# Performance work log

Measured on AMD Instinct MI355X. Metric: run time of the kernel, lower is better.

The kernel has to match this reference:

```python
import jax, jax.numpy as jnp
import numpy as np
import math

D_MODEL = 1024
NUM_HEADS = 16
HEAD_DIM = D_MODEL // NUM_HEADS
BATCH = 2
SEQ = 2048
THETA = 10000.0


def _rope_tables(seq_len, head_dim, theta=THETA):
    inv_freq = 1.0 / theta ** (jnp.arange(0, head_dim, 2, dtype=jnp.float32) / head_dim)
    pos = jnp.arange(seq_len, dtype=jnp.float32)
    freqs = jnp.outer(pos, inv_freq)                 # [S, hd/2]
    emb = jnp.concatenate([freqs, freqs], axis=-1)   # [S, hd]
    return jnp.cos(emb), jnp.sin(emb)


def _rotate_half(x):
    x1, x2 = jnp.split(x, 2, axis=-1)
    return jnp.concatenate([-x2, x1], axis=-1)


def setup_inputs() -> dict:
    key = jax.random.key(0)
    k1, k2, k3 = jax.random.split(key, 3)
    x = jax.random.normal(k1, (BATCH, SEQ, D_MODEL), dtype=jnp.float32)
    # causal mask: 1 where attend allowed, 0 where masked
    mask = jnp.tril(jnp.ones((SEQ, SEQ), dtype=jnp.int32))[None, None]
    w_qkv = jax.random.normal(k2, (D_MODEL, 3 * D_MODEL), dtype=jnp.float32) / math.sqrt(D_MODEL)
    w_out = jax.random.normal(k3, (D_MODEL, D_MODEL), dtype=jnp.float32) / math.sqrt(D_MODEL)
    return {"x": x, "mask": mask, "w_qkv": w_qkv, "w_out": w_out}


def reference(x, mask, w_qkv, w_out):
    B, S, _ = x.shape
    qkv = x @ w_qkv                                          # [B,S,3*D]
    qkv = qkv.reshape(B, S, 3, NUM_HEADS, HEAD_DIM)
    qkv = jnp.transpose(qkv, (2, 0, 3, 1, 4))                # [3,B,H,S,hd]
    q, k, v = qkv[0], qkv[1], qkv[2]
    cos, sin = _rope_tables(S, HEAD_DIM)                     # [S,hd]
    cos = cos[None, None]; sin = sin[None, None]
    q = q * cos + _rotate_half(q) * sin
    k = k * cos + _rotate_half(k) * sin
    scores = jnp.einsum('bhqd,bhkd->bhqk', q, k) / math.sqrt(HEAD_DIM)
    scores = jnp.where(mask == 0, -jnp.inf, scores)
    attn = jax.nn.softmax(scores, axis=-1)                   # dropout p=0 (eval)
    out = jnp.einsum('bhqk,bhkd->bhqd', attn, v)             # [B,H,S,hd]
    out = jnp.transpose(out, (0, 2, 1, 3)).reshape(B, S, D_MODEL)
    return out @ w_out
```

## Files before the change

### kernel.cpp

```cpp
#include <hip/hip_runtime.h>

typedef __bf16 bf16;
typedef __bf16 bf16x4 __attribute__((ext_vector_type(4)));
typedef __bf16 bf16x8 __attribute__((ext_vector_type(8)));
typedef short s16x4 __attribute__((ext_vector_type(4)));
typedef float f32x4 __attribute__((ext_vector_type(4)));

constexpr int BATCH = 2;
constexpr int SEQ   = 2048;
constexpr int DMODEL= 1024;
constexpr int NH    = 16;
constexpr int HD    = 64;
constexpr int M_ROWS= BATCH * SEQ;
constexpr int N_QKV = 3 * DMODEL;

#if defined(__HIP_DEVICE_COMPILE__) && __has_builtin(__builtin_amdgcn_exp2f)
#define EXP2(x) __builtin_amdgcn_exp2f(x)
#else
#define EXP2(x) exp2f(x)
#endif

__device__ __forceinline__ void gl_lds16(const bf16* g, bf16* l) {
  __builtin_amdgcn_global_load_lds(
      (const __attribute__((address_space(1))) unsigned int*)g,
      (__attribute__((address_space(3))) unsigned int*)l, 16, 0, 0);
}

__device__ __forceinline__ f32x4 mfma_16x16x16_bf16(bf16x4 a, bf16x4 b,
                                                    f32x4 c) {
#if defined(__HIP_DEVICE_COMPILE__)
  union { bf16x4 h; s16x4 s; } ua{a}, ub{b};
  return __builtin_amdgcn_mfma_f32_16x16x16bf16_1k(ua.s, ub.s, c, 0, 0, 0);
#else
  return c;
#endif
}

__global__ __launch_bounds__(256) void prep_kernel(
    const float* __restrict__ x, const float* __restrict__ w_qkv,
    const float* __restrict__ w_out, bf16* __restrict__ xb,
    bf16* __restrict__ WqkvT, bf16* __restrict__ WoutT) {
  const int bx = blockIdx.x, t = threadIdx.x;
  if (bx < 2048) {
    const int i = (bx * 256 + t) * 8;
    float4 f0 = *(const float4*)&x[i];
    float4 f1 = *(const float4*)&x[i + 4];
    bf16x8 v;
    v[0] = (bf16)f0.x; v[1] = (bf16)f0.y; v[2] = (bf16)f0.z; v[3] = (bf16)f0.w;
    v[4] = (bf16)f1.x; v[5] = (bf16)f1.y; v[6] = (bf16)f1.z; v[7] = (bf16)f1.w;
    *(bf16x8*)&xb[i] = v;
    return;
  }
  __shared__ float tile[32][33];
  const float* src;
  bf16* dst;
  int R, C, c0, r0;
  if (bx < 5120) {
    const int idx = bx - 2048;
    src = w_qkv; dst = WqkvT; R = DMODEL; C = N_QKV;
    c0 = (idx % 96) * 32; r0 = (idx / 96) * 32;
  } else {
    const int idx = bx - 5120;
    src = w_out; dst = WoutT; R = DMODEL; C = DMODEL;
    c0 = (idx & 31) * 32; r0 = (idx >> 5) * 32;
  }
  const int r = t >> 3, c4 = (t & 7) * 4;
  {
    float4 f = *(const float4*)&src[(size_t)(r0 + r) * C + c0 + c4];
    tile[r][c4 + 0] = f.x; tile[r][c4 + 1] = f.y;
    tile[r][c4 + 2] = f.z; tile[r][c4 + 3] = f.w;
  }
  __syncthreads();
  {
    bf16x4 v;
#pragma unroll
    for (int j = 0; j < 4; j++) v[j] = (bf16)tile[c4 + j][r];
    *(bf16x4*)&dst[(size_t)(c0 + r) * R + r0 + c4] = v;
  }
}

__global__ __launch_bounds__(256) void gemm_out64(
    const bf16* __restrict__ A, const bf16* __restrict__ BT,
    float* __restrict__ C, int M, int N, int K) {
  __shared__ bf16 As[64 * 32];
  __shared__ bf16 Bs[128 * 32];
  const int t = threadIdx.x;
  const int m0 = blockIdx.y * 64;
  const int n0 = blockIdx.x * 128;
  const int w = t >> 6, lane = t & 63, g = lane >> 4, li = lane & 15;
  const int r0w = (w & 1) * 32, c0w = (w >> 1) * 64;
  f32x4 acc[2][4] = {};
  for (int k0 = 0; k0 < K; k0 += 32) {
    __syncthreads();
    {
      const int idx = w * 64 + lane;
      const int row = idx >> 2, col = (idx & 3) * 8;
      gl_lds16(&A[(size_t)(m0 + row) * K + k0 + col], &As[w * 512]);
    }
#pragma unroll
    for (int c = 0; c < 2; c++) {
      const int idx = (w * 2 + c) * 64 + lane;
      const int row = idx >> 2, col = (idx & 3) * 8;
      gl_lds16(&BT[(size_t)(n0 + row) * K + k0 + col], &Bs[(w * 2 + c) * 512]);
    }
    __syncthreads();
    bf16x8 a[2], b[4];
#pragma unroll
    for (int mt = 0; mt < 2; mt++)
      a[mt] = *(const bf16x8*)&As[(r0w + mt * 16 + li) * 32 + g * 8];
#pragma unroll
    for (int nt = 0; nt < 4; nt++)
      b[nt] = *(const bf16x8*)&Bs[(c0w + nt * 16 + li) * 32 + g * 8];
#pragma unroll
    for (int mt = 0; mt < 2; mt++)
#pragma unroll
      for (int nt = 0; nt < 4; nt++)
        acc[mt][nt] = __builtin_amdgcn_mfma_f32_16x16x32_bf16(
            a[mt], b[nt], acc[mt][nt], 0, 0, 0);
  }
#pragma unroll
  for (int mt = 0; mt < 2; mt++)
#pragma unroll
    for (int nt = 0; nt < 4; nt++)
#pragma unroll
      for (int r = 0; r < 4; r++) {
        const int m = m0 + r0w + mt * 16 + g * 4 + r;
        const int n = n0 + c0w + nt * 16 + li;
        C[(size_t)m * N + n] = acc[mt][nt][r];
      }
}

__global__ __launch_bounds__(256) void gemm_qkv_rope(
    const bf16* __restrict__ A, const bf16* __restrict__ BT,
    bf16* __restrict__ Qb, bf16* __restrict__ Kb, bf16* __restrict__ Vt) {
  constexpr int K = DMODEL;
  __shared__ bf16 smem[16384];
  const int t = threadIdx.x;
  const int bid = blockIdx.x;
  const int swz = (bid & 7) * 96 + (bid >> 3);
  const int m0 = (swz & 31) * 128;
  const int n0 = (swz >> 5) * 128;
  const int w = t >> 6, lane = t & 63, g = lane >> 4, li = lane & 15;
  const int r0w = (w & 1) * 64, c0w = (w >> 1) * 64;
  f32x4 acc[4][4] = {};

  const int i0 = (w * 2 + 0) * 64 + lane, i1 = (w * 2 + 1) * 64 + lane;
  const int sr0 = i0 >> 2, sc0 = (i0 & 3) * 8;
  const int sr1 = i1 >> 2, sc1 = (i1 & 3) * 8;

#define QKV_STAGE(buf, k0)                                                   \
  {                                                                          \
    bf16* Asb = smem + (buf)*4096;                                           \
    bf16* Bsb = smem + 8192 + (buf)*4096;                                    \
    gl_lds16(&A[(size_t)(m0 + sr0) * K + (k0) + sc0],                        \
             &Asb[(w * 2 + 0) * 512]);                                       \
    gl_lds16(&A[(size_t)(m0 + sr1) * K + (k0) + sc1],                        \
             &Asb[(w * 2 + 1) * 512]);                                       \
    gl_lds16(&BT[(size_t)(n0 + sr0) * K + (k0) + sc0],                       \
             &Bsb[(w * 2 + 0) * 512]);                                       \
    gl_lds16(&BT[(size_t)(n0 + sr1) * K + (k0) + sc1],                       \
             &Bsb[(w * 2 + 1) * 512]);                                       \
  }

  QKV_STAGE(0, 0);
  __syncthreads();
  for (int it = 0; it < 32; ++it) {
    const int cur = it & 1;
    if (it < 31) QKV_STAGE(cur ^ 1, (it + 1) * 32);
    const bf16* Asb = smem + cur * 4096;
    const bf16* Bsb = smem + 8192 + cur * 4096;
    bf16x8 a[4], b[4];
#pragma unroll
    for (int mt = 0; mt < 4; mt++)
      a[mt] = *(const bf16x8*)&Asb[(r0w + mt * 16 + li) * 32 + g * 8];
#pragma unroll
    for (int nt = 0; nt < 4; nt++)
      b[nt] = *(const bf16x8*)&Bsb[(c0w + nt * 16 + li) * 32 + g * 8];
#pragma unroll
    for (int mt = 0; mt < 4; mt++)
#pragma unroll
      for (int nt = 0; nt < 4; nt++)
        acc[mt][nt] = __builtin_amdgcn_mfma_f32_16x16x32_bf16(
            a[mt], b[nt], acc[mt][nt], 0, 0, 0);
    __syncthreads();
  }
#undef QKV_STAGE

  const int region = n0 >> 10;
  const int b = m0 >> 11;
  const int h = ((n0 + c0w) >> 6) & 15;
  const size_t bh = (size_t)(b * NH + h);

  if (region < 2) {
    bf16* dst = region == 0 ? Qb : Kb;
    const float outsc = region == 0 ? 0.125f * 1.44269504f : 1.f;
    const float L = 13.287712379549449f;
    const float if0 = exp2f(-(float)(2 * li) / 64.f * L);
    const float if1 = exp2f(-(float)(2 * (li + 16)) / 64.f * L);
    bf16* lw = smem + w * 2112;
#pragma unroll
    for (int pass = 0; pass < 2; pass++) {
      __syncthreads();
#pragma unroll
      for (int mtl = 0; mtl < 2; mtl++) {
        const int mt = pass * 2 + mtl;
#pragma unroll
        for (int r = 0; r < 4; r++) {
          const int s = (m0 + r0w + mt * 16 + g * 4 + r) & (SEQ - 1);
          float cs[2], sn[2];
          __sincosf((float)s * if0, &sn[0], &cs[0]);
          __sincosf((float)s * if1, &sn[1], &cs[1]);
#pragma unroll
          for (int nt = 0; nt < 4; nt++) {
            const int par = nt & 1;
            const float a = acc[mt][nt][r];
            const float ap = acc[mt][nt ^ 2][r];
            const float v = (nt < 2) ? a * cs[par] - ap * sn[par]
                                     : a * cs[par] + ap * sn[par];
            lw[(mtl * 16 + g * 4 + r) * 66 + nt * 16 + li] =
                (bf16)(v * outsc);
          }
        }
      }
      __syncthreads();
      const int rowl = lane >> 1, dh = (lane & 1) * 32;
      const int s = (m0 + r0w + pass * 32 + rowl) & (SEQ - 1);
      bf16* gdst = &dst[(bh * SEQ + s) * HD + dh];
      const bf16* lsrc = &lw[rowl * 66 + dh];
#pragma unroll
      for (int c = 0; c < 4; c++)
        *(bf16x8*)&gdst[c * 8] = *(const bf16x8*)&lsrc[c * 8];
    }
  } else {
#pragma unroll
    for (int mt = 0; mt < 4; mt++)
#pragma unroll
      for (int nt = 0; nt < 4; nt++) {
        const int s = (m0 + r0w + mt * 16 + g * 4) & (SEQ - 1);
        const int d = nt * 16 + li;
        bf16x4 v;
#pragma unroll
        for (int r = 0; r < 4; r++) v[r] = (bf16)acc[mt][nt][r];
        *(bf16x4*)&Vt[(bh * HD + d) * SEQ + s] = v;
      }
  }
}

__device__ const unsigned char CHUNK_TAB[80] = {
    124, 125, 126, 127,
    120, 121, 122, 116, 117, 118, 112, 113, 114, 108, 109, 110,
    104, 105, 106, 100, 101, 102, 96,  97,  98,  92,  93,  94,
    88,  89,  84,  85,  80,  81,  76,  77,  72,  73,  68,  69,
    64,  65,  60,  61,
    56,  52,  48,  44,  40,  36,  32,  28,
    24,  57,  90,  123, 20,  53,  86,  119, 16,  49,  82,  115,
    12,  45,  78,  111, 8,   41,  74,  107, 4,   37,  70,  103,
    0,   33,  66,  99};

__global__ __launch_bounds__(256, 5) void flash_attn15(
    const bf16* __restrict__ Q, const bf16* __restrict__ Kb,
    const bf16* __restrict__ Vt, bf16* __restrict__ Oout,
    float* __restrict__ Opart, float* __restrict__ Lpart) {
  const int bx = blockIdx.x;
  const unsigned char e = CHUNK_TAB[bx >> 5];
  const int qt = e >> 2, kch = e & 3;
  const int bh = bx & 31;
  const int q0 = qt * 64;
  const int jlo = kch * 8;
  const int jhi = min(jlo + 8, qt + 1);
  const int t = threadIdx.x, w = t >> 6, lane = t & 63, g = lane >> 4,
            li = lane & 15;

  __shared__ bf16 Ks[2][4096];
  __shared__ bf16 Vs[2][4096];

  const bf16* Qh = Q  + (size_t)bh * SEQ * HD;
  const bf16* Kh = Kb + (size_t)bh * SEQ * HD;
  const bf16* Vh = Vt + (size_t)bh * HD * SEQ;

  const int qw = q0 + w * 16;

  bf16x8 qf[2];
#pragma unroll
  for (int ks = 0; ks < 2; ks++)
    qf[ks] = *(const bf16x8*)&Qh[(size_t)(qw + li) * HD + ks * 32 + g * 8];

  f32x4 o[4] = {};
  f32x4 o4  = {};
  bf16x4 ones;
#pragma unroll
  for (int r = 0; r < 4; r++) ones[r] = (bf16)1.f;

  int koffB[2][4];
#pragma unroll
  for (int ks = 0; ks < 2; ks++)
#pragma unroll
    for (int nt = 0; nt < 4; nt++) {
      const int rK = nt * 16 + li;
      const int pK = rK * 8 + ((ks * 4 + g) ^ (li & 7));
      koffB[ks][nt] = pK * 16;
    }
  int voffB[4][4];
#pragma unroll
  for (int nt = 0; nt < 4; nt++)
#pragma unroll
    for (int dt = 0; dt < 4; dt++) {
      const int rV = dt * 16 + li;
      const int cg = nt * 2 + (g >> 1);
      const int pV = rV * 8 + (cg ^ (rV & 7));
      voffB[nt][dt] = pV * 16 + (g & 1) * 8;
    }

  const int p0 = w * 128 + lane, p1 = p0 + 64;
  const int sr0 = p0 >> 3, sc0 = ((p0 & 7) ^ (sr0 & 7)) * 8;
  const int sr1 = p1 >> 3, sc1 = ((p1 & 7) ^ (sr1 & 7)) * 8;
  const int lo0 = w * 1024, lo1 = w * 1024 + 512;

  {
    const int jn = jlo * 64;
    gl_lds16(&Kh[(size_t)(jn + sr0) * HD + sc0], &Ks[jlo & 1][lo0]);
    gl_lds16(&Kh[(size_t)(jn + sr1) * HD + sc1], &Ks[jlo & 1][lo1]);
    gl_lds16(&Vh[(size_t)sr0 * SEQ + jn + sc0], &Vs[jlo & 1][lo0]);
    gl_lds16(&Vh[(size_t)sr1 * SEQ + jn + sc1], &Vs[jlo & 1][lo1]);
  }
  __syncthreads();

  for (int ti = jlo; ti < jhi; ++ti) {
    const int cur = ti & 1, nxt = cur ^ 1;
    const char* ksb = (const char*)&Ks[cur][0];
    const char* vsb = (const char*)&Vs[cur][0];
    if (ti + 1 < jhi) {
      const int jn = ti * 64 + 64;
      gl_lds16(&Kh[(size_t)(jn + sr0) * HD + sc0], &Ks[nxt][lo0]);
      gl_lds16(&Kh[(size_t)(jn + sr1) * HD + sc1], &Ks[nxt][lo1]);
      gl_lds16(&Vh[(size_t)sr0 * SEQ + jn + sc0], &Vs[nxt][lo0]);
      gl_lds16(&Vh[(size_t)sr1 * SEQ + jn + sc1], &Vs[nxt][lo1]);
    }

    if (ti < qt) {
      f32x4 sacc[4] = {};
      __builtin_amdgcn_s_setprio(1);
#pragma unroll
      for (int ks = 0; ks < 2; ks++)
#pragma unroll
        for (int nt = 0; nt < 4; nt++) {
          bf16x8 kf = *(const bf16x8*)(ksb + koffB[ks][nt]);
          sacc[nt] = __builtin_amdgcn_mfma_f32_16x16x32_bf16(kf, qf[ks],
                                                             sacc[nt], 0, 0, 0);
        }
      __builtin_amdgcn_s_setprio(0);

      bf16x4 pf[4];
#pragma unroll
      for (int nt = 0; nt < 4; nt++)
#pragma unroll
        for (int r = 0; r < 4; r++) pf[nt][r] = (bf16)EXP2(sacc[nt][r]);

      __builtin_amdgcn_s_setprio(1);
#pragma unroll
      for (int nt = 0; nt < 4; nt++) {
        o4 = mfma_16x16x16_bf16(ones, pf[nt], o4);
#pragma unroll
        for (int dt = 0; dt < 4; dt++) {
          bf16x4 vfrag = *(const bf16x4*)(vsb + voffB[nt][dt]);
          o[dt] = mfma_16x16x16_bf16(vfrag, pf[nt], o[dt]);
        }
      }
      __builtin_amdgcn_s_setprio(0);
    } else {
      f32x4 sacc[4] = {};
      __builtin_amdgcn_s_setprio(1);
#pragma unroll
      for (int ks = 0; ks < 2; ks++)
#pragma unroll
        for (int nt = 0; nt < 4; nt++) {
          if (nt > w) continue;
          bf16x8 kf = *(const bf16x8*)(ksb + koffB[ks][nt]);
          sacc[nt] = __builtin_amdgcn_mfma_f32_16x16x32_bf16(kf, qf[ks],
                                                             sacc[nt], 0, 0, 0);
        }
      __builtin_amdgcn_s_setprio(0);

      bf16x4 pf[4];
#pragma unroll
      for (int nt = 0; nt < 4; nt++) {
        if (nt > w) continue;
#pragma unroll
        for (int r = 0; r < 4; r++) {
          float v = sacc[nt][r];
          if (nt == w) {
            const int kk = nt * 16 + g * 4 + r;
            v = (kk <= w * 16 + li) ? v : -1e30f;
          }
          pf[nt][r] = (bf16)EXP2(v);
        }
      }

      __builtin_amdgcn_s_setprio(1);
#pragma unroll
      for (int nt = 0; nt < 4; nt++) {
        if (nt > w) continue;
        o4 = mfma_16x16x16_bf16(ones, pf[nt], o4);
#pragma unroll
        for (int dt = 0; dt < 4; dt++) {
          bf16x4 vfrag = *(const bf16x4*)(vsb + voffB[nt][dt]);
          o[dt] = mfma_16x16x16_bf16(vfrag, pf[nt], o[dt]);
        }
      }
      __builtin_amdgcn_s_setprio(0);
    }
    __syncthreads();
  }

  if (qt <= 7) {
    const float inv_l = 1.f / o4[0];
    const int b = bh >> 4, h = bh & 15;
    const int s = qw + li;
#pragma unroll
    for (int dt = 0; dt < 4; dt++) {
      bf16x4 ov;
#pragma unroll
      for (int r = 0; r < 4; r++) ov[r] = (bf16)(o[dt][r] * inv_l);
      *(bf16x4*)&Oout[((size_t)(b * SEQ + s)) * DMODEL + h * 64 + dt * 16 +
                      g * 4] = ov;
    }
  } else {
    const int s = qw + li;
    int off;
    if (qt < 16)       off = (s - 512) * 2 + kch;
    else if (qt < 24)  off = 1024 + (s - 1024) * 3 + kch;
    else               off = 2560 + (s - 1536) * 4 + kch;
    const size_t slot = (size_t)bh * 4608 + off;
    if (g == 0) Lpart[slot] = o4[0];
    float* od = &Opart[slot * 64];
#pragma unroll
    for (int dt = 0; dt < 4; dt++)
      *(f32x4*)&od[dt * 16 + g * 4] = o[dt];
  }
}

__global__ __launch_bounds__(256) void attn_merge2(
    const float* __restrict__ Opart, const float* __restrict__ Lpart,
    bf16* __restrict__ attn) {
  const int gi = blockIdx.x * 256 + threadIdx.x;
  const int row = gi >> 3;
  const int d0 = (gi & 7) * 8;
  const int bh = row / 1536, srel = row - bh * 1536;
  const int b = bh >> 4, h = bh & 15, s = srel + 512;
  int off0, nc;
  if (srel < 512)       { off0 = srel * 2;                nc = 2; }
  else if (srel < 1024) { off0 = 1024 + (srel - 512) * 3; nc = 3; }
  else                  { off0 = 2560 + (srel - 1024) * 4; nc = 4; }
  const size_t base = (size_t)bh * 4608 + off0;
  float lsum = 0.f;
  float acc[8] = {};
  for (int c = 0; c < nc; c++) {
    lsum += Lpart[base + c];
    const float* p = &Opart[(base + c) * 64 + d0];
    float4 a0 = *(const float4*)p;
    float4 a1 = *(const float4*)(p + 4);
    acc[0] += a0.x; acc[1] += a0.y; acc[2] += a0.z; acc[3] += a0.w;
    acc[4] += a1.x; acc[5] += a1.y; acc[6] += a1.z; acc[7] += a1.w;
  }
  const float inv = 1.f / lsum;
  bf16x8 v;
#pragma unroll
  for (int i = 0; i < 8; i++) v[i] = (bf16)(acc[i] * inv);
  *(bf16x8*)&attn[((size_t)(b * SEQ + s)) * DMODEL + h * 64 + d0] = v;
}

extern "C" void kernel_launch(void* const* d_in, const int* in_sizes, int n_in,
                              void* d_out, int out_size, void* d_ws,
                              size_t ws_size, hipStream_t stream) {
  const float* x     = (const float*)d_in[0];
  const float* w_qkv = (const float*)d_in[2];
  const float* w_out = (const float*)d_in[3];
  float* out = (float*)d_out;

  char* ws = (char*)d_ws;
  bf16* WqkvT = (bf16*)(ws);
  bf16* WoutT = (bf16*)(ws + 6291456);
  bf16* xb    = (bf16*)(ws + 8388608);
  bf16* Qb    = (bf16*)(ws + 16777216);
  bf16* Kbuf  = (bf16*)(ws + 25165824);
  bf16* Vt    = (bf16*)(ws + 33554432);
  bf16* attn  = (bf16*)(ws + 41943040);
  float* Opart= (float*)(ws + 50331648);
  float* Lpart= (float*)(ws + 88080384);

  prep_kernel<<<dim3(6144), 256, 0, stream>>>(x, w_qkv, w_out, xb, WqkvT,
                                              WoutT);
  gemm_qkv_rope<<<dim3(768), 256, 0, stream>>>(xb, WqkvT, Qb, Kbuf, Vt);
  flash_attn15<<<dim3(2560), 256, 0, stream>>>(Qb, Kbuf, Vt, attn, Opart,
                                               Lpart);
  attn_merge2<<<dim3(1536), 256, 0, stream>>>(Opart, Lpart, attn);
  gemm_out64<<<dim3(DMODEL / 128, M_ROWS / 64), 256, 0, stream>>>(
      attn, WoutT, out, M_ROWS, DMODEL, DMODEL);
}
```

Measured before the change: 191.9 us.

## Enlarge flash-attention query tile to 128 rows with 8 waves per block

```diff
diff --git a/kernel.cpp b/kernel.cpp
--- a/kernel.cpp
+++ b/kernel.cpp
@@ -246,30 +246,28 @@
   }
 }
 
-__device__ const unsigned char CHUNK_TAB[80] = {
-    124, 125, 126, 127,
-    120, 121, 122, 116, 117, 118, 112, 113, 114, 108, 109, 110,
-    104, 105, 106, 100, 101, 102, 96,  97,  98,  92,  93,  94,
-    88,  89,  84,  85,  80,  81,  76,  77,  72,  73,  68,  69,
-    64,  65,  60,  61,
-    56,  52,  48,  44,  40,  36,  32,  28,
-    24,  57,  90,  123, 20,  53,  86,  119, 16,  49,  82,  115,
-    12,  45,  78,  111, 8,   41,  74,  107, 4,   37,  70,  103,
-    0,   33,  66,  99};
-
-__global__ __launch_bounds__(256, 5) void flash_attn15(
+__device__ const unsigned char CHUNK_TAB17[40] = {
+    63, 62, 61, 60, 58, 57, 56, 54, 53, 52, 50, 49, 48, 46, 45, 44,
+    41, 40, 37, 36, 33, 32, 29, 28, 24, 20, 16, 12,
+    59, 42, 25, 8,
+    55, 38, 21, 4,
+    51, 34, 17, 0};
+
+__global__ __launch_bounds__(512, 8) void flash_attn17(
     const bf16* __restrict__ Q, const bf16* __restrict__ Kb,
     const bf16* __restrict__ Vt, bf16* __restrict__ Oout,
     float* __restrict__ Opart, float* __restrict__ Lpart) {
   const int bx = blockIdx.x;
-  const unsigned char e = CHUNK_TAB[bx >> 5];
+  const unsigned char e = CHUNK_TAB17[bx >> 5];
   const int qt = e >> 2, kch = e & 3;
   const int bh = bx & 31;
-  const int q0 = qt * 64;
+  const int q0 = qt * 128;
   const int jlo = kch * 8;
-  const int jhi = min(jlo + 8, qt + 1);
+  const int jhi = min(jlo + 8, 2 * qt + 2);
   const int t = threadIdx.x, w = t >> 6, lane = t & 63, g = lane >> 4,
             li = lane & 15;
+  const int mw = w & 3;
+  const int diagw = 2 * qt + (w >> 2);
 
   __shared__ bf16 Ks[2][4096];
   __shared__ bf16 Vs[2][4096];
@@ -311,17 +309,14 @@
       voffB[nt][dt] = pV * 16 + (g & 1) * 8;
     }
 
-  const int p0 = w * 128 + lane, p1 = p0 + 64;
-  const int sr0 = p0 >> 3, sc0 = ((p0 & 7) ^ (sr0 & 7)) * 8;
-  const int sr1 = p1 >> 3, sc1 = ((p1 & 7) ^ (sr1 & 7)) * 8;
-  const int lo0 = w * 1024, lo1 = w * 1024 + 512;
+  const int p = w * 64 + lane;
+  const int sr = p >> 3, sc = ((p & 7) ^ (sr & 7)) * 8;
+  const int lo = w * 512;
 
   {
     const int jn = jlo * 64;
-    gl_lds16(&Kh[(size_t)(jn + sr0) * HD + sc0], &Ks[jlo & 1][lo0]);
-    gl_lds16(&Kh[(size_t)(jn + sr1) * HD + sc1], &Ks[jlo & 1][lo1]);
-    gl_lds16(&Vh[(size_t)sr0 * SEQ + jn + sc0], &Vs[jlo & 1][lo0]);
-    gl_lds16(&Vh[(size_t)sr1 * SEQ + jn + sc1], &Vs[jlo & 1][lo1]);
+    gl_lds16(&Kh[(size_t)(jn + sr) * HD + sc], &Ks[jlo & 1][lo]);
+    gl_lds16(&Vh[(size_t)sr * SEQ + jn + sc], &Vs[jlo & 1][lo]);
   }
   __syncthreads();
 
@@ -331,13 +326,11 @@
     const char* vsb = (const char*)&Vs[cur][0];
     if (ti + 1 < jhi) {
       const int jn = ti * 64 + 64;
-      gl_lds16(&Kh[(size_t)(jn + sr0) * HD + sc0], &Ks[nxt][lo0]);
-      gl_lds16(&Kh[(size_t)(jn + sr1) * HD + sc1], &Ks[nxt][lo1]);
-      gl_lds16(&Vh[(size_t)sr0 * SEQ + jn + sc0], &Vs[nxt][lo0]);
-      gl_lds16(&Vh[(size_t)sr1 * SEQ + jn + sc1], &Vs[nxt][lo1]);
-    }
-
-    if (ti < qt) {
+      gl_lds16(&Kh[(size_t)(jn + sr) * HD + sc], &Ks[nxt][lo]);
+      gl_lds16(&Vh[(size_t)sr * SEQ + jn + sc], &Vs[nxt][lo]);
+    }
+
+    if (ti < diagw) {
       f32x4 sacc[4] = {};
       __builtin_amdgcn_s_setprio(1);
 #pragma unroll
@@ -367,14 +360,14 @@
         }
       }
       __builtin_amdgcn_s_setprio(0);
-    } else {
+    } else if (ti == diagw) {
       f32x4 sacc[4] = {};
       __builtin_amdgcn_s_setprio(1);
 #pragma unroll
       for (int ks = 0; ks < 2; ks++)
 #pragma unroll
         for (int nt = 0; nt < 4; nt++) {
-          if (nt > w) continue;
+          if (nt > mw) continue;
           bf16x8 kf = *(const bf16x8*)(ksb + koffB[ks][nt]);
           sacc[nt] = __builtin_amdgcn_mfma_f32_16x16x32_bf16(kf, qf[ks],
                                                              sacc[nt], 0, 0, 0);
@@ -384,13 +377,13 @@
       bf16x4 pf[4];
 #pragma unroll
       for (int nt = 0; nt < 4; nt++) {
-        if (nt > w) continue;
+        if (nt > mw) continue;
 #pragma unroll
         for (int r = 0; r < 4; r++) {
           float v = sacc[nt][r];
-          if (nt == w) {
+          if (nt == mw) {
             const int kk = nt * 16 + g * 4 + r;
-            v = (kk <= w * 16 + li) ? v : -1e30f;
+            v = (kk <= mw * 16 + li) ? v : -1e30f;
           }
           pf[nt][r] = (bf16)EXP2(v);
         }
@@ -399,7 +392,7 @@
       __builtin_amdgcn_s_setprio(1);
 #pragma unroll
       for (int nt = 0; nt < 4; nt++) {
-        if (nt > w) continue;
+        if (nt > mw) continue;
         o4 = mfma_16x16x16_bf16(ones, pf[nt], o4);
 #pragma unroll
         for (int dt = 0; dt < 4; dt++) {
@@ -412,7 +405,7 @@
     __syncthreads();
   }
 
-  if (qt <= 7) {
+  if (qt <= 3) {
     const float inv_l = 1.f / o4[0];
     const int b = bh >> 4, h = bh & 15;
     const int s = qw + li;
@@ -427,8 +420,8 @@
   } else {
     const int s = qw + li;
     int off;
-    if (qt < 16)       off = (s - 512) * 2 + kch;
-    else if (qt < 24)  off = 1024 + (s - 1024) * 3 + kch;
+    if (qt < 8)        off = (s - 512) * 2 + kch;
+    else if (qt < 12)  off = 1024 + (s - 1024) * 3 + kch;
     else               off = 2560 + (s - 1536) * 4 + kch;
     const size_t slot = (size_t)bh * 4608 + off;
     if (g == 0) Lpart[slot] = o4[0];
@@ -491,7 +484,7 @@
   prep_kernel<<<dim3(6144), 256, 0, stream>>>(x, w_qkv, w_out, xb, WqkvT,
                                               WoutT);
   gemm_qkv_rope<<<dim3(768), 256, 0, stream>>>(xb, WqkvT, Qb, Kbuf, Vt);
-  flash_attn15<<<dim3(2560), 256, 0, stream>>>(Qb, Kbuf, Vt, attn, Opart,
+  flash_attn17<<<dim3(1280), 512, 0, stream>>>(Qb, Kbuf, Vt, attn, Opart,
                                                Lpart);
   attn_merge2<<<dim3(1536), 256, 0, stream>>>(Opart, Lpart, attn);
   gemm_out64<<<dim3(DMODEL / 128, M_ROWS / 64), 256, 0, stream>>>(
```

Result: slower. 203.6 us (+6.1%).
